# Performance work log

Measured on AMD Instinct MI355X. Metric: run time of the kernel, lower is better.

Reference implementation:

```python
import jax, jax.numpy as jnp
import numpy as np

H_HEADS = 16
STATE_N = 64

def setup_inputs() -> dict:
    key = jax.random.key(0)
    ks = jax.random.split(key, 9)
    B, T, D = 2, 1024, 1024
    H, ch, N = H_HEADS, D // H_HEADS, STATE_N
    inp = jax.random.normal(ks[0], (B, T, D), dtype=jnp.float32)
    # lin_logA params scaled so exp(cumsum(logA)) stays bounded (decaying state)
    W_logA = jax.random.normal(ks[1], (H, 1, ch), dtype=jnp.float32) * 0.01
    b_logA = jnp.full((H, 1), -0.05, dtype=jnp.float32)
    W_XBC = jax.random.normal(ks[3], (H, ch + 2 * N, ch), dtype=jnp.float32) * (1.0 / np.sqrt(ch))
    b_XBC = jax.random.normal(ks[4], (H, ch + 2 * N), dtype=jnp.float32) * 0.02
    W_gate = jax.random.normal(ks[5], (H, ch, ch), dtype=jnp.float32) * (1.0 / np.sqrt(ch))
    b_gate = jax.random.normal(ks[6], (H, ch), dtype=jnp.float32) * 0.02
    W_out = jax.random.normal(ks[7], (D, D), dtype=jnp.float32) * (1.0 / np.sqrt(D))
    b_out = jax.random.normal(ks[8], (D,), dtype=jnp.float32) * 0.02
    return {"inp": inp, "W_logA": W_logA, "b_logA": b_logA, "W_XBC": W_XBC,
            "b_XBC": b_XBC, "W_gate": W_gate, "b_gate": b_gate,
            "W_out": W_out, "b_out": b_out}

def _mamba2_forward(inp, W_logA, b_logA, W_XBC, b_XBC, W_gate, b_gate, W_out, b_out):
    B, T, D = inp.shape
    H, N = H_HEADS, STATE_N
    ch = D // H
    x = inp.reshape(B, T, H, ch)  # B,T,H,ch
    # MultiheadLinear: matmul((H,out,in), x[...,None]) + bias
    logA = jnp.einsum('hoc,bthc->btho', W_logA, x)[..., 0] + b_logA[:, 0]  # B,T,H
    XBC = jax.nn.silu(jnp.einsum('hoc,bthc->btho', W_XBC, x) + b_XBC)     # B,T,H,ch+2N
    X = XBC[..., :ch]                 # B,T,H,ch
    Bm = XBC[..., ch:ch + N]          # B,T,H,N
    Cm = XBC[..., ch + N:]            # B,T,H,N
    # quadratic SSM: A_ss[b,h,i,j] = exp(cum[i]-cum[j]) for j<=i else 0
    cum = jnp.cumsum(jnp.swapaxes(logA, 1, 2), axis=-1)  # B,H,T
    diff = cum[..., :, None] - cum[..., None, :]          # B,H,T,T
    causal = jnp.tril(jnp.ones((T, T), dtype=bool))
    A_ss = jnp.where(causal, jnp.exp(jnp.where(causal, diff, 0.0)), 0.0)  # B,H,T,T
    G = jnp.einsum('bihn,bjhn->bhij', Cm, Bm)             # B,H,T,T (C_i . B_j)
    Y = jnp.einsum('bhij,bjhc->bihc', A_ss * G, X)        # B,T,H,ch
    gate = jnp.einsum('hoc,bthc->btho', W_gate, x) + b_gate
    Yg = (gate * Y).reshape(B, T, D)
    return Yg @ W_out.T + b_out

def reference(inp, W_logA, b_logA, W_XBC, b_XBC, W_gate, b_gate, W_out, b_out):
    return _mamba2_forward(inp, W_logA, b_logA, W_XBC, b_XBC, W_gate, b_gate, W_out, b_out)
```

## Files before the change

kernel.cpp:

```cpp
#include <hip/hip_runtime.h>

typedef unsigned int   u32;
typedef unsigned short u16;
typedef __attribute__((ext_vector_type(8))) short bf16x8;
typedef __attribute__((ext_vector_type(4))) float f32x4;

__device__ __forceinline__ float bfs(u16 u) {
  union { u32 i; float f; } v; v.i = ((u32)u) << 16; return v.f;
}
__device__ __forceinline__ u16 f2bf(float f) {
  union { float f; u32 i; } v; v.f = f;
  u32 r = v.i + 0x7fffu + ((v.i >> 16) & 1u);
  return (u16)(r >> 16);
}
__device__ __forceinline__ ushort4 f2bf4(float4 v) {
  ushort4 p; p.x = f2bf(v.x); p.y = f2bf(v.y); p.z = f2bf(v.z); p.w = f2bf(v.w);
  return p;
}

__global__ __launch_bounds__(256) void k_proj(
    const float* __restrict__ inp,
    const float* __restrict__ W_XBC,  const float* __restrict__ b_XBC,
    const float* __restrict__ W_gate, const float* __restrict__ b_gate,
    const float* __restrict__ W_logA, const float* __restrict__ b_logA,
    const float* __restrict__ Wout, u16* __restrict__ WoutB,
    u16* __restrict__ XsT, u16* __restrict__ BmsT, u16* __restrict__ CmsT,
    u16* __restrict__ gatesP, float* __restrict__ lexp, float* __restrict__ linv,
    float* __restrict__ decArr, float* __restrict__ G)
{
  int tt = blockIdx.x, h = blockIdx.y;
  int tid = threadIdx.x;
  int w = tid >> 6, l = tid & 63, q = l >> 4, lr = l & 15;
  int m0 = tt * 64;
  int b = m0 >> 10, tl0 = m0 & 1023;
  int bh = b * 16 + h;
  int jt = tt & 15;

  __shared__ u16 Xt[64][72];
  __shared__ u16 Wt[256][72];
  __shared__ float wl[64];
  __shared__ float sg[64];

  {
    int fid = h * 32 + tt;
    const float4* src = (const float4*)Wout + (size_t)fid * 512;
    ushort4* dst = (ushort4*)WoutB + (size_t)fid * 512;
    for (int i = tid; i < 512; i += 256) dst[i] = f2bf4(src[i]);
  }

  if (tid < 64) wl[tid] = W_logA[h * 64 + tid];
#pragma unroll
  for (int i = 0; i < 4; ++i) {
    int f = tid + 256 * i; int r = f >> 4, cq = f & 15;
    float4 xv = *(const float4*)(inp + (size_t)(m0 + r) * 1024 + h * 64 + 4 * cq);
    *(ushort4*)&Xt[r][4 * cq] = f2bf4(xv);
  }
#pragma unroll
  for (int i = 0; i < 16; ++i) {
    int f = tid + 256 * i; int r = f >> 4, cq = f & 15;
    const float* ws = (r < 192) ? (W_XBC + ((size_t)h * 192 + r) * 64)
                                : (W_gate + ((size_t)h * 64 + (r - 192)) * 64);
    *(ushort4*)&Wt[r][4 * cq] = f2bf4(*(const float4*)(ws + 4 * cq));
  }
  __syncthreads();

  bf16x8 af[4][2];
#pragma unroll
  for (int rt = 0; rt < 4; ++rt) {
    af[rt][0] = *(const bf16x8*)&Xt[16 * rt + lr][q * 8];
    af[rt][1] = *(const bf16x8*)&Xt[16 * rt + lr][32 + q * 8];
  }

  f32x4 acc[4][4];
#pragma unroll
  for (int rt = 0; rt < 4; ++rt)
#pragma unroll
    for (int ct = 0; ct < 4; ++ct) acc[rt][ct] = (f32x4){0.f, 0.f, 0.f, 0.f};

#pragma unroll
  for (int ct = 0; ct < 4; ++ct) {
    bf16x8 b0 = *(const bf16x8*)&Wt[64 * w + 16 * ct + lr][q * 8];
    bf16x8 b1 = *(const bf16x8*)&Wt[64 * w + 16 * ct + lr][32 + q * 8];
#pragma unroll
    for (int rt = 0; rt < 4; ++rt) {
      acc[rt][ct] = __builtin_amdgcn_mfma_f32_16x16x32_bf16(af[rt][0], b0, acc[rt][ct], 0, 0, 0);
      acc[rt][ct] = __builtin_amdgcn_mfma_f32_16x16x32_bf16(af[rt][1], b1, acc[rt][ct], 0, 0, 0);
    }
  }

  if (tid < 64) {
    float a = b_logA[h];
#pragma unroll 16
    for (int k = 0; k < 64; ++k) a += bfs(Xt[tid][k]) * wl[k];
    float lv = a;
#pragma unroll
    for (int off = 1; off < 64; off <<= 1) {
      float n = __shfl_up(lv, off, 64);
      if (tid >= off) lv += n;
    }
    float L = __shfl(lv, 63, 64);
    sg[tid] = __expf(L - lv);
    lexp[(size_t)bh * 1024 + tl0 + tid] = __expf(lv);
    linv[(size_t)bh * 1024 + tl0 + tid] = __expf(-lv);
    if (tid == 63) decArr[bh * 16 + jt] = __expf(L);
  }

  if (w < 3) {
#pragma unroll
    for (int ct = 0; ct < 4; ++ct) {
      float bias = b_XBC[h * 192 + 64 * w + 16 * ct + lr];
#pragma unroll
      for (int rt = 0; rt < 4; ++rt)
#pragma unroll
        for (int r = 0; r < 4; ++r) {
          float s = acc[rt][ct][r] + bias;
          acc[rt][ct][r] = s / (1.f + __expf(-s));
        }
    }
  } else {
#pragma unroll
    for (int ct = 0; ct < 4; ++ct) {
      float bias = b_gate[h * 64 + 16 * ct + lr];
#pragma unroll
      for (int rt = 0; rt < 4; ++rt)
#pragma unroll
        for (int r = 0; r < 4; ++r) acc[rt][ct][r] += bias;
    }
  }
  __syncthreads();

  {
    u16* T = &Wt[64 * w][0];
#pragma unroll
    for (int ct = 0; ct < 4; ++ct)
#pragma unroll
      for (int rt = 0; rt < 4; ++rt)
#pragma unroll
        for (int r = 0; r < 4; ++r) {
          int t = 16 * rt + 4 * q + r, n = 16 * ct + lr;
          u16 v = f2bf(acc[rt][ct][r]);
          if (w < 3) T[n * 72 + t] = v;
          else       T[t * 72 + n] = v;
        }
  }
  __syncthreads();

  {
#pragma unroll
    for (int i = 0; i < 16; ++i) {
      int s = l + 64 * i; int row = s >> 4, cq = s & 15;
      ushort4 v = *(ushort4*)&Wt[64 * w + row][4 * cq];
      if (w == 0)
        *(ushort4*)(XsT + ((size_t)bh * 64 + row) * 1024 + tl0 + 4 * cq) = v;
      else if (w == 1)
        *(ushort4*)(BmsT + ((size_t)bh * 64 + row) * 1024 + tl0 + 4 * cq) = v;
      else if (w == 2)
        *(ushort4*)(CmsT + ((size_t)bh * 64 + row) * 1024 + tl0 + 4 * cq) = v;
      else
        *(ushort4*)(gatesP + ((size_t)bh * 1024 + tl0 + row) * 64 + 4 * cq) = v;
    }
  }

  {
    bf16x8 a0r = *(const bf16x8*)&Wt[16 * w + lr][q * 8];
    bf16x8 a1r = *(const bf16x8*)&Wt[16 * w + lr][32 + q * 8];
    bf16x8 a0, a1;
#pragma unroll
    for (int jj = 0; jj < 8; ++jj) {
      a0[jj] = (short)f2bf(bfs((u16)a0r[jj]) * sg[q * 8 + jj]);
      a1[jj] = (short)f2bf(bfs((u16)a1r[jj]) * sg[32 + q * 8 + jj]);
    }
    f32x4 gacc[4];
#pragma unroll
    for (int nt = 0; nt < 4; ++nt) {
      gacc[nt] = (f32x4){0.f, 0.f, 0.f, 0.f};
      bf16x8 bb0 = *(const bf16x8*)&Wt[64 + 16 * nt + lr][q * 8];
      bf16x8 bb1 = *(const bf16x8*)&Wt[64 + 16 * nt + lr][32 + q * 8];
      gacc[nt] = __builtin_amdgcn_mfma_f32_16x16x32_bf16(a0, bb0, gacc[nt], 0, 0, 0);
      gacc[nt] = __builtin_amdgcn_mfma_f32_16x16x32_bf16(a1, bb1, gacc[nt], 0, 0, 0);
    }
    float* Gt = G + ((size_t)bh * 16 + jt) * 4096;
#pragma unroll
    for (int nt = 0; nt < 4; ++nt)
#pragma unroll
      for (int r = 0; r < 4; ++r)
        Gt[(16 * w + 4 * q + r) * 64 + 16 * nt + lr] = gacc[nt][r];
  }
}

__global__ __launch_bounds__(1024) void k_mid(
    const float* __restrict__ G, const float* __restrict__ decArr,
    u16* __restrict__ HpreT)
{
  int cc = blockIdx.x, bh = blockIdx.y;
  int tid = threadIdx.x;
  int e = cc * 1024 + tid;
  __shared__ float dsm[16];
  if (tid < 16) dsm[tid] = decArr[bh * 16 + tid];
  __syncthreads();
  const float* Gb = G + (size_t)bh * 16 * 4096 + e;
  float g[16];
#pragma unroll
  for (int jtl = 0; jtl < 16; ++jtl) g[jtl] = Gb[(size_t)jtl * 4096];
  u16* Hb = HpreT + (size_t)bh * 16 * 4096 + e;
  float hst = 0.f;
#pragma unroll
  for (int jtl = 0; jtl < 16; ++jtl) {
    Hb[(size_t)jtl * 4096] = f2bf(hst);
    hst = dsm[jtl] * hst + g[jtl];
  }
}

__global__ __launch_bounds__(256) void k_ssm2(
    const u16* __restrict__ XsT, const u16* __restrict__ BmsT,
    const u16* __restrict__ CmsT,
    const float* __restrict__ lexp, const float* __restrict__ linv,
    const u16* __restrict__ HpreT, const u16* __restrict__ gatesP,
    u16* __restrict__ Yg)
{
  int it = blockIdx.x, bh = blockIdx.y;
  int b = bh >> 4, h = bh & 15;
  int tid = threadIdx.x;
  int w = tid >> 6, l = tid & 63, q = l >> 4, lr = l & 15;
  int i0 = it * 64;

  __shared__ u16 Cts[64][72];
  __shared__ u16 Bts[64][72];
  __shared__ u16 Xts[64][72];
  __shared__ u16 HTt[64][72];
  __shared__ u16 Gts[64][72];
  __shared__ u16 Sts[64][72];
  __shared__ float ref_[64], cef[64];

  const u16* Xb  = XsT  + (size_t)bh * 64 * 1024;
  const u16* BbT = BmsT + (size_t)bh * 64 * 1024;
  const u16* CbT = CmsT + (size_t)bh * 64 * 1024;
  const u16* Hb  = HpreT + ((size_t)bh * 16 + it) * 4096;
  const u16* Gb  = gatesP + ((size_t)bh * 1024 + i0) * 64;

#pragma unroll
  for (int i = 0; i < 4; ++i) {
    int f = tid + 256 * i; int r = f >> 4, cq = f & 15;
    *(ushort4*)&Xts[r][4 * cq] = *(const ushort4*)(Xb + (size_t)r * 1024 + i0 + 4 * cq);
    *(ushort4*)&HTt[r][4 * cq] = *(const ushort4*)(Hb + r * 64 + 4 * cq);
    *(ushort4*)&Gts[r][4 * cq] = *(const ushort4*)(Gb + r * 64 + 4 * cq);
    ushort4 bv = *(const ushort4*)(BbT + (size_t)r * 1024 + i0 + 4 * cq);
    Bts[4 * cq + 0][r] = bv.x; Bts[4 * cq + 1][r] = bv.y;
    Bts[4 * cq + 2][r] = bv.z; Bts[4 * cq + 3][r] = bv.w;
    ushort4 cv = *(const ushort4*)(CbT + (size_t)r * 1024 + i0 + 4 * cq);
    Cts[4 * cq + 0][r] = cv.x; Cts[4 * cq + 1][r] = cv.y;
    Cts[4 * cq + 2][r] = cv.z; Cts[4 * cq + 3][r] = cv.w;
  }
  if (tid < 64) {
    ref_[tid] = lexp[(size_t)bh * 1024 + i0 + tid];
    cef[tid]  = linv[(size_t)bh * 1024 + i0 + tid];
  }
  __syncthreads();

  bf16x8 ca0 = *(const bf16x8*)&Cts[16 * w + lr][q * 8];
  bf16x8 ca1 = *(const bf16x8*)&Cts[16 * w + lr][32 + q * 8];

#pragma unroll
  for (int ct = 0; ct < 4; ++ct) {
    f32x4 s = (f32x4){0.f, 0.f, 0.f, 0.f};
    bf16x8 b0 = *(const bf16x8*)&Bts[16 * ct + lr][q * 8];
    bf16x8 b1 = *(const bf16x8*)&Bts[16 * ct + lr][32 + q * 8];
    s = __builtin_amdgcn_mfma_f32_16x16x32_bf16(ca0, b0, s, 0, 0, 0);
    s = __builtin_amdgcn_mfma_f32_16x16x32_bf16(ca1, b1, s, 0, 0, 0);
    int jl = 16 * ct + lr;
    float cj = cef[jl];
#pragma unroll
    for (int r = 0; r < 4; ++r) {
      int il = 16 * w + q * 4 + r;
      float v = (jl > il) ? 0.f : s[r] * ref_[il] * cj;
      Sts[il][jl] = f2bf(v);
    }
  }

  bf16x8 sa0 = *(const bf16x8*)&Sts[16 * w + lr][q * 8];
  bf16x8 sa1 = *(const bf16x8*)&Sts[16 * w + lr][32 + q * 8];
  f32x4 accd[4], acco[4];
#pragma unroll
  for (int ct = 0; ct < 4; ++ct) {
    accd[ct] = (f32x4){0.f, 0.f, 0.f, 0.f};
    acco[ct] = (f32x4){0.f, 0.f, 0.f, 0.f};
    bf16x8 x0 = *(const bf16x8*)&Xts[16 * ct + lr][q * 8];
    bf16x8 x1 = *(const bf16x8*)&Xts[16 * ct + lr][32 + q * 8];
    accd[ct] = __builtin_amdgcn_mfma_f32_16x16x32_bf16(sa0, x0, accd[ct], 0, 0, 0);
    accd[ct] = __builtin_amdgcn_mfma_f32_16x16x32_bf16(sa1, x1, accd[ct], 0, 0, 0);
    bf16x8 h0 = *(const bf16x8*)&HTt[16 * ct + lr][q * 8];
    bf16x8 h1 = *(const bf16x8*)&HTt[16 * ct + lr][32 + q * 8];
    acco[ct] = __builtin_amdgcn_mfma_f32_16x16x32_bf16(ca0, h0, acco[ct], 0, 0, 0);
    acco[ct] = __builtin_amdgcn_mfma_f32_16x16x32_bf16(ca1, h1, acco[ct], 0, 0, 0);
  }

#pragma unroll
  for (int ct = 0; ct < 4; ++ct) {
    int c = 16 * ct + lr;
#pragma unroll
    for (int r = 0; r < 4; ++r) {
      int il = 16 * w + q * 4 + r;
      int tg = i0 + il;
      size_t row = (size_t)(b * 1024 + tg);
      float y = accd[ct][r] + ref_[il] * acco[ct][r];
      float gt = bfs(Gts[il][c]);
      Yg[row * 1024 + h * 64 + c] = f2bf(y * gt);
    }
  }
}

__global__ __launch_bounds__(512) void k_out(
    const u16* __restrict__ Yg, const u16* __restrict__ WoutB,
    const float* __restrict__ bout, float* __restrict__ out)
{
  int bm = blockIdx.x, bn = blockIdx.y;
  int tid = threadIdx.x;
  int w = tid >> 6, l = tid & 63, q = l >> 4, lr = l & 15;
  int m0 = bm * 128, d0 = bn * 64;

  __shared__ u16 Yt[128][72];
  __shared__ u16 Wt[64][72];

  f32x4 acc[4];
#pragma unroll
  for (int ct = 0; ct < 4; ++ct) acc[ct] = (f32x4){0.f, 0.f, 0.f, 0.f};

  ushort4 py[4], pw[2];
#pragma unroll
  for (int i = 0; i < 4; ++i) {
    int f = tid + 512 * i; int r = f >> 4, cq = f & 15;
    py[i] = *(const ushort4*)(Yg + (size_t)(m0 + r) * 1024 + 4 * cq);
  }
#pragma unroll
  for (int i = 0; i < 2; ++i) {
    int f = tid + 512 * i; int r = f >> 4, cq = f & 15;
    pw[i] = *(const ushort4*)(WoutB + (size_t)(d0 + r) * 1024 + 4 * cq);
  }

  for (int kt = 0; kt < 16; ++kt) {
    __syncthreads();
#pragma unroll
    for (int i = 0; i < 4; ++i) {
      int f = tid + 512 * i; int r = f >> 4, cq = f & 15;
      *(ushort4*)&Yt[r][4 * cq] = py[i];
    }
#pragma unroll
    for (int i = 0; i < 2; ++i) {
      int f = tid + 512 * i; int r = f >> 4, cq = f & 15;
      *(ushort4*)&Wt[r][4 * cq] = pw[i];
    }
    __syncthreads();

    if (kt < 15) {
      int k1 = (kt + 1) * 64;
#pragma unroll
      for (int i = 0; i < 4; ++i) {
        int f = tid + 512 * i; int r = f >> 4, cq = f & 15;
        py[i] = *(const ushort4*)(Yg + (size_t)(m0 + r) * 1024 + k1 + 4 * cq);
      }
#pragma unroll
      for (int i = 0; i < 2; ++i) {
        int f = tid + 512 * i; int r = f >> 4, cq = f & 15;
        pw[i] = *(const ushort4*)(WoutB + (size_t)(d0 + r) * 1024 + k1 + 4 * cq);
      }
    }

    bf16x8 a0 = *(const bf16x8*)&Yt[16 * w + lr][q * 8];
    bf16x8 a1 = *(const bf16x8*)&Yt[16 * w + lr][32 + q * 8];
#pragma unroll
    for (int ct = 0; ct < 4; ++ct) {
      bf16x8 b0 = *(const bf16x8*)&Wt[16 * ct + lr][q * 8];
      bf16x8 b1 = *(const bf16x8*)&Wt[16 * ct + lr][32 + q * 8];
      acc[ct] = __builtin_amdgcn_mfma_f32_16x16x32_bf16(a0, b0, acc[ct], 0, 0, 0);
      acc[ct] = __builtin_amdgcn_mfma_f32_16x16x32_bf16(a1, b1, acc[ct], 0, 0, 0);
    }
  }

#pragma unroll
  for (int ct = 0; ct < 4; ++ct) {
    int d = d0 + 16 * ct + lr;
    float bo = bout[d];
#pragma unroll
    for (int r = 0; r < 4; ++r) {
      int m = m0 + 16 * w + q * 4 + r;
      out[(size_t)m * 1024 + d] = acc[ct][r] + bo;
    }
  }
}

extern "C" void kernel_launch(void* const* d_in, const int* in_sizes, int n_in,
                              void* d_out, int out_size, void* d_ws, size_t ws_size,
                              hipStream_t stream)
{
  const float* inp   = (const float*)d_in[0];
  const float* WlogA = (const float*)d_in[1];
  const float* blogA = (const float*)d_in[2];
  const float* WXBC  = (const float*)d_in[3];
  const float* bXBC  = (const float*)d_in[4];
  const float* Wgate = (const float*)d_in[5];
  const float* bgate = (const float*)d_in[6];
  const float* Wout  = (const float*)d_in[7];
  const float* bout  = (const float*)d_in[8];
  float* out = (float*)d_out;

  const size_t SZ = (size_t)2 * 16 * 1024 * 64;
  float* lexp   = (float*)d_ws;
  float* linv   = lexp + 32768;
  float* decA   = linv + 32768;
  float* G      = decA + 512;
  u16* base16 = (u16*)(G + (size_t)32 * 16 * 4096);
  u16* XsT    = base16;
  u16* BmsT   = XsT + SZ;
  u16* CmsT   = BmsT + SZ;
  u16* gatesP = CmsT + SZ;
  u16* Yg     = gatesP + SZ;
  u16* WoutB  = Yg + SZ;
  u16* HpreT  = WoutB + 1024 * 1024;

  k_proj<<<dim3(32, 16), 256, 0, stream>>>(inp, WXBC, bXBC, Wgate, bgate,
                                           WlogA, blogA, Wout, WoutB,
                                           XsT, BmsT, CmsT, gatesP,
                                           lexp, linv, decA, G);
  k_mid<<<dim3(4, 32), 1024, 0, stream>>>(G, decA, HpreT);
  k_ssm2<<<dim3(16, 32), 256, 0, stream>>>(XsT, BmsT, CmsT, lexp, linv,
                                           HpreT, gatesP, Yg);
  k_out<<<dim3(16, 16), 512, 0, stream>>>(Yg, WoutB, bout, out);
}
```

Measured before the change: 118.4 us.

## Store B/C time-major and stage gated Y output through LDS for coalesced writes

k_proj now writes the B and C projections in time-major (row, 64-channel) layout, using an extra LDS tile. This lets k_ssm2 load them with vector LDS stores instead of scalar transposing writes. k_ssm2 also drops its gate LDS tile and stages Y through LDS, then applies the gate and writes Yg with coalesced ushort4 stores instead of scattered 2-byte stores. In exchange there is extra LDS use and an extra barrier, and Y is rounded to bf16 before the gate multiply, which adds a second rounding step.

```diff
diff --git a/kernel.cpp b/kernel.cpp
--- a/kernel.cpp
+++ b/kernel.cpp
@@ -24,7 +24,7 @@
     const float* __restrict__ W_gate, const float* __restrict__ b_gate,
     const float* __restrict__ W_logA, const float* __restrict__ b_logA,
     const float* __restrict__ Wout, u16* __restrict__ WoutB,
-    u16* __restrict__ XsT, u16* __restrict__ BmsT, u16* __restrict__ CmsT,
+    u16* __restrict__ XsT, u16* __restrict__ Bms, u16* __restrict__ Cms,
     u16* __restrict__ gatesP, float* __restrict__ lexp, float* __restrict__ linv,
     float* __restrict__ decArr, float* __restrict__ G)
 {
@@ -38,6 +38,7 @@
 
   __shared__ u16 Xt[64][72];
   __shared__ u16 Wt[256][72];
+  __shared__ u16 Wt2[128][72];
   __shared__ float wl[64];
   __shared__ float sg[64];
 
@@ -130,7 +131,6 @@
   __syncthreads();
 
   {
-    u16* T = &Wt[64 * w][0];
 #pragma unroll
     for (int ct = 0; ct < 4; ++ct)
 #pragma unroll
@@ -139,8 +139,16 @@
         for (int r = 0; r < 4; ++r) {
           int t = 16 * rt + 4 * q + r, n = 16 * ct + lr;
           u16 v = f2bf(acc[rt][ct][r]);
-          if (w < 3) T[n * 72 + t] = v;
-          else       T[t * 72 + n] = v;
+          if (w == 0) {
+            Wt[n][t] = v;
+          } else if (w == 1) {
+            Wt[64 + n][t] = v;
+            Wt2[t][n] = v;
+          } else if (w == 2) {
+            Wt2[64 + t][n] = v;
+          } else {
+            Wt[192 + t][n] = v;
+          }
         }
   }
   __syncthreads();
@@ -149,15 +157,19 @@
 #pragma unroll
     for (int i = 0; i < 16; ++i) {
       int s = l + 64 * i; int row = s >> 4, cq = s & 15;
-      ushort4 v = *(ushort4*)&Wt[64 * w + row][4 * cq];
-      if (w == 0)
+      if (w == 0) {
+        ushort4 v = *(ushort4*)&Wt[row][4 * cq];
         *(ushort4*)(XsT + ((size_t)bh * 64 + row) * 1024 + tl0 + 4 * cq) = v;
-      else if (w == 1)
-        *(ushort4*)(BmsT + ((size_t)bh * 64 + row) * 1024 + tl0 + 4 * cq) = v;
-      else if (w == 2)
-        *(ushort4*)(CmsT + ((size_t)bh * 64 + row) * 1024 + tl0 + 4 * cq) = v;
-      else
+      } else if (w == 1) {
+        ushort4 v = *(ushort4*)&Wt2[row][4 * cq];
+        *(ushort4*)(Bms + ((size_t)bh * 1024 + tl0 + row) * 64 + 4 * cq) = v;
+      } else if (w == 2) {
+        ushort4 v = *(ushort4*)&Wt2[64 + row][4 * cq];
+        *(ushort4*)(Cms + ((size_t)bh * 1024 + tl0 + row) * 64 + 4 * cq) = v;
+      } else {
+        ushort4 v = *(ushort4*)&Wt[192 + row][4 * cq];
         *(ushort4*)(gatesP + ((size_t)bh * 1024 + tl0 + row) * 64 + 4 * cq) = v;
+      }
     }
   }
 
@@ -212,8 +224,8 @@
 }
 
 __global__ __launch_bounds__(256) void k_ssm2(
-    const u16* __restrict__ XsT, const u16* __restrict__ BmsT,
-    const u16* __restrict__ CmsT,
+    const u16* __restrict__ XsT, const u16* __restrict__ Bms,
+    const u16* __restrict__ Cms,
     const float* __restrict__ lexp, const float* __restrict__ linv,
     const u16* __restrict__ HpreT, const u16* __restrict__ gatesP,
     u16* __restrict__ Yg)
@@ -228,28 +240,22 @@
   __shared__ u16 Bts[64][72];
   __shared__ u16 Xts[64][72];
   __shared__ u16 HTt[64][72];
-  __shared__ u16 Gts[64][72];
   __shared__ u16 Sts[64][72];
   __shared__ float ref_[64], cef[64];
 
-  const u16* Xb  = XsT  + (size_t)bh * 64 * 1024;
-  const u16* BbT = BmsT + (size_t)bh * 64 * 1024;
-  const u16* CbT = CmsT + (size_t)bh * 64 * 1024;
-  const u16* Hb  = HpreT + ((size_t)bh * 16 + it) * 4096;
-  const u16* Gb  = gatesP + ((size_t)bh * 1024 + i0) * 64;
+  const u16* Xb = XsT + (size_t)bh * 64 * 1024;
+  const u16* Bb = Bms + (size_t)bh * 64 * 1024;
+  const u16* Cb = Cms + (size_t)bh * 64 * 1024;
+  const u16* Hb = HpreT + ((size_t)bh * 16 + it) * 4096;
+  const u16* Gb = gatesP + ((size_t)bh * 1024 + i0) * 64;
 
 #pragma unroll
   for (int i = 0; i < 4; ++i) {
     int f = tid + 256 * i; int r = f >> 4, cq = f & 15;
     *(ushort4*)&Xts[r][4 * cq] = *(const ushort4*)(Xb + (size_t)r * 1024 + i0 + 4 * cq);
     *(ushort4*)&HTt[r][4 * cq] = *(const ushort4*)(Hb + r * 64 + 4 * cq);
-    *(ushort4*)&Gts[r][4 * cq] = *(const ushort4*)(Gb + r * 64 + 4 * cq);
-    ushort4 bv = *(const ushort4*)(BbT + (size_t)r * 1024 + i0 + 4 * cq);
-    Bts[4 * cq + 0][r] = bv.x; Bts[4 * cq + 1][r] = bv.y;
-    Bts[4 * cq + 2][r] = bv.z; Bts[4 * cq + 3][r] = bv.w;
-    ushort4 cv = *(const ushort4*)(CbT + (size_t)r * 1024 + i0 + 4 * cq);
-    Cts[4 * cq + 0][r] = cv.x; Cts[4 * cq + 1][r] = cv.y;
-    Cts[4 * cq + 2][r] = cv.z; Cts[4 * cq + 3][r] = cv.w;
+    *(ushort4*)&Bts[r][4 * cq] = *(const ushort4*)(Bb + (size_t)(i0 + r) * 64 + 4 * cq);
+    *(ushort4*)&Cts[r][4 * cq] = *(const ushort4*)(Cb + (size_t)(i0 + r) * 64 + 4 * cq);
   }
   if (tid < 64) {
     ref_[tid] = lexp[(size_t)bh * 1024 + i0 + tid];
@@ -294,18 +300,31 @@
     acco[ct] = __builtin_amdgcn_mfma_f32_16x16x32_bf16(ca1, h1, acco[ct], 0, 0, 0);
   }
 
+  __syncthreads();
+
 #pragma unroll
   for (int ct = 0; ct < 4; ++ct) {
     int c = 16 * ct + lr;
 #pragma unroll
     for (int r = 0; r < 4; ++r) {
       int il = 16 * w + q * 4 + r;
-      int tg = i0 + il;
-      size_t row = (size_t)(b * 1024 + tg);
       float y = accd[ct][r] + ref_[il] * acco[ct][r];
-      float gt = bfs(Gts[il][c]);
-      Yg[row * 1024 + h * 64 + c] = f2bf(y * gt);
-    }
+      Xts[il][c] = f2bf(y);
+    }
+  }
+  __syncthreads();
+
+#pragma unroll
+  for (int i = 0; i < 4; ++i) {
+    int f = tid + 256 * i; int r = f >> 4, cq = f & 15;
+    ushort4 yv = *(ushort4*)&Xts[r][4 * cq];
+    ushort4 gv = *(const ushort4*)(Gb + (size_t)r * 64 + 4 * cq);
+    ushort4 o;
+    o.x = f2bf(bfs(yv.x) * bfs(gv.x));
+    o.y = f2bf(bfs(yv.y) * bfs(gv.y));
+    o.z = f2bf(bfs(yv.z) * bfs(gv.z));
+    o.w = f2bf(bfs(yv.w) * bfs(gv.w));
+    *(ushort4*)(Yg + ((size_t)(b * 1024 + i0 + r)) * 1024 + h * 64 + 4 * cq) = o;
   }
 }
 
@@ -410,19 +429,19 @@
   float* G      = decA + 512;
   u16* base16 = (u16*)(G + (size_t)32 * 16 * 4096);
   u16* XsT    = base16;
-  u16* BmsT   = XsT + SZ;
-  u16* CmsT   = BmsT + SZ;
-  u16* gatesP = CmsT + SZ;
+  u16* Bms    = XsT + SZ;
+  u16* Cms    = Bms + SZ;
+  u16* gatesP = Cms + SZ;
   u16* Yg     = gatesP + SZ;
   u16* WoutB  = Yg + SZ;
   u16* HpreT  = WoutB + 1024 * 1024;
 
   k_proj<<<dim3(32, 16), 256, 0, stream>>>(inp, WXBC, bXBC, Wgate, bgate,
                                            WlogA, blogA, Wout, WoutB,
-                                           XsT, BmsT, CmsT, gatesP,
+                                           XsT, Bms, Cms, gatesP,
                                            lexp, linv, decA, G);
   k_mid<<<dim3(4, 32), 1024, 0, stream>>>(G, decA, HpreT);
-  k_ssm2<<<dim3(16, 32), 256, 0, stream>>>(XsT, BmsT, CmsT, lexp, linv,
+  k_ssm2<<<dim3(16, 32), 256, 0, stream>>>(XsT, Bms, Cms, lexp, linv,
                                            HpreT, gatesP, Yg);
   k_out<<<dim3(16, 16), 512, 0, stream>>>(Yg, WoutB, bout, out);
 }
```

Result: slower. 124.7 us (+5.3%).
